# Performance work log

Measured on AMD Instinct MI355X. Metric: run time of the kernel, lower is better.

The kernel has to match this reference:

```python
import jax, jax.numpy as jnp
import numpy as np

K = 27        # num_neighs
EPS = 1e-5    # BatchNorm eps (torch default)
LATENT = 256


def _knn_idx(pts, k):
    # pts: (B, N, 3) -> (B, N, k) indices of k nearest points (self included, dist 0),
    # matching torch_cluster.knn(x, x, k).
    d = jnp.sum((pts[:, :, None, :] - pts[:, None, :, :]) ** 2, axis=-1)  # (B, N, N)
    _, idx = jax.lax.top_k(-d, k)
    return idx


def _graph_feature(x, idx):
    # x: (B, C, N), idx: (B, N, K) -> (B, 2C, N, K) = concat(neigh - center, center)
    xt = jnp.transpose(x, (0, 2, 1))               # (B, N, C)
    neigh = jax.vmap(lambda p, i: p[i])(xt, idx)   # (B, N, K, C) gather
    center = xt[:, :, None, :]                     # (B, N, 1, C)
    feat = jnp.concatenate([neigh - center, jnp.broadcast_to(center, neigh.shape)], axis=-1)
    return jnp.transpose(feat, (0, 3, 1, 2))       # (B, 2C, N, K)


def _bn_lrelu(x, gamma, beta, axes):
    # Training-mode BatchNorm (biased batch stats over `axes`, channel = dim 1) + LeakyReLU(0.2)
    mean = jnp.mean(x, axis=axes, keepdims=True)
    var = jnp.var(x, axis=axes, keepdims=True)
    shape = [1] * x.ndim
    shape[1] = -1
    y = (x - mean) * jax.lax.rsqrt(var + EPS) * gamma.reshape(shape) + beta.reshape(shape)
    return jnp.where(y >= 0, y, 0.2 * y)


def setup_inputs() -> dict:
    key = jax.random.key(0)
    ks = jax.random.split(key, 6)
    B, T, N = 2, 2, 256
    x = jax.random.normal(ks[0], (B, T, N, 3), dtype=jnp.float32)
    # Conv2d(1x1) channel ladder for depth=4, bb_size=24, input_features=6
    dims = [(6, 48), (192, 192), (768, 768), (3072, 3072)]
    inp = {"x": x}
    for i, (cin, cout) in enumerate(dims):
        inp[f"w{i}"] = jax.random.normal(ks[i + 1], (cout, cin), dtype=jnp.float32) * 0.05
        inp[f"g{i}"] = jnp.ones((cout,), jnp.float32)
        inp[f"b{i}"] = jnp.zeros((cout,), jnp.float32)
    # final Conv1d(8160 -> latent): 8160 = 48*(2+8+32+128)
    inp["w4"] = jax.random.normal(ks[5], (LATENT, 8160), dtype=jnp.float32) * 0.02
    inp["g4"] = jnp.ones((LATENT,), jnp.float32)
    inp["b4"] = jnp.zeros((LATENT,), jnp.float32)
    return inp


def reference(x, w0, g0, b0, w1, g1, b1, w2, g2, b2, w3, g3, b3, w4, g4, b4):
    B, T, N, _ = x.shape
    flat = x.reshape(B * T, N, 3)
    idx = _knn_idx(flat, K)  # fixed neighbors reused at every depth (only_true_neighs=True)
    cur = _graph_feature(jnp.transpose(flat, (0, 2, 1)), idx)  # (BT, 6, N, K)
    outs = []
    for w, g, b in [(w0, g0, b0), (w1, g1, b1), (w2, g2, b2), (w3, g3, b3)]:
        if outs:
            cur = _graph_feature(outs[-1], idx)      # (BT, 2C_prev, N, K)
        h = jnp.einsum('bcnk,oc->bonk', cur, w)      # 1x1 conv, no bias
        h = _bn_lrelu(h, g, b, axes=(0, 2, 3))
        hmax = jnp.max(h, axis=-1)                   # max over K neighbors -> (BT, C, N)
        C = hmax.shape[1]
        exp = hmax.reshape(B, T, C, N)
        # Faithful to source: avgpool does `out, _ = x.mean(dim=1, keepdim=True)` which
        # tuple-unpacks the batch dim (requires B==2): out = batch-0 temporal mean (1, C, N),
        # then expanded to (B, T, C, N).
        tp = jnp.mean(exp, axis=1, keepdims=True)[0]  # (1, C, N)
        comb = jnp.concatenate([exp, jnp.broadcast_to(tp[None], exp.shape)], axis=2)  # (B,T,2C,N)
        outs.append(comb.reshape(B * T, 2 * C, N))
    xcat = jnp.concatenate(outs, axis=1)             # (BT, 8160, N)
    y = jnp.einsum('bcn,oc->bon', xcat, w4)          # 1x1 conv1d
    y = _bn_lrelu(y, g4, b4, axes=(0, 2))
    return y.reshape(B, T, LATENT, N)
```

## Files before the change

kernel.cpp:

```cpp
#include <hip/hip_runtime.h>
#include <hip/hip_bf16.h>

#define NPTS 256
#define NB   4
#define KNN  27
#define EPSV 1e-5f

typedef unsigned short u16;
typedef _Float16 f16;
typedef __attribute__((ext_vector_type(8))) _Float16 f16x8;
typedef __attribute__((ext_vector_type(4))) _Float16 f16x4;
typedef __attribute__((ext_vector_type(4))) float f32x4;

#define OFF_IDX    0
#define OFF_XYZ    131072
#define OFF_A0     262144
#define OFF_A1     270336
#define OFF_A2     344064
#define OFF_A3     1523712
#define OFF_A4     20398080
#define OFF_PQ     24576000
#define OFF_SLICE  74907648
#define OFF_XC     100073472
#define OFF_Y      116785152

typedef __attribute__((address_space(3))) unsigned int lds_u32_t;
typedef __attribute__((address_space(1))) unsigned int glb_u32_t;

__device__ __forceinline__ void gload16(const f16* g, const u16* l) {
    __builtin_amdgcn_global_load_lds((const glb_u32_t*)g, (lds_u32_t*)(u16*)l, 16, 0, 0);
}

__device__ __forceinline__ float dist3_nocontract(float ax, float ay, float az,
                                                  float bx, float by, float bz) {
#pragma clang fp contract(off)
    float dx = bx - ax, dy = by - ay, dz = bz - az;
    float s = dx * dx;
    s = s + dy * dy;
    s = s + dz * dz;
    return s;
}

__global__ __launch_bounds__(256) void knn_prep(
    const float* __restrict__ x, int* __restrict__ idx, f16* __restrict__ xyz,
    const float* __restrict__ w0, const float* __restrict__ w1,
    const float* __restrict__ w2, const float* __restrict__ w3,
    const float* __restrict__ w4, char* __restrict__ ws)
{
    int bid = blockIdx.x;
    int tid = threadIdx.x;

    if (bid < 256) {
        int wid = tid >> 6;
        int lane = tid & 63;
        int pt = bid * 4 + wid;
        int b = pt >> 8, n = pt & 255;

        float xp0 = x[pt * 3 + 0];
        float xp1 = x[pt * 3 + 1];
        float xp2 = x[pt * 3 + 2];

        if (lane < 32) {
            float v = (lane < 3) ? x[pt * 3 + lane] : 0.f;
            xyz[((long)b * NPTS + n) * 32 + lane] = (f16)v;
        }

        unsigned long long key[4];
#pragma unroll
        for (int u = 0; u < 4; ++u) {
            int j = lane + 64 * u;
            int gj = b * NPTS + j;
            float d = dist3_nocontract(xp0, xp1, xp2,
                                       x[gj * 3 + 0], x[gj * 3 + 1], x[gj * 3 + 2]);
            key[u] = ((unsigned long long)__float_as_uint(d) << 32) | (unsigned int)j;
        }

        for (int r = 0; r < KNN; ++r) {
            unsigned long long m = key[0];
            m = key[1] < m ? key[1] : m;
            m = key[2] < m ? key[2] : m;
            m = key[3] < m ? key[3] : m;
#pragma unroll
            for (int off = 32; off; off >>= 1) {
                unsigned long long o = __shfl_xor(m, off);
                m = o < m ? o : m;
            }
            if (lane == 0) idx[pt * 28 + r] = (int)(m & 0xffffffffu);
#pragma unroll
            for (int u = 0; u < 4; ++u)
                if (key[u] == m) key[u] = ~0ULL;
        }
        return;
    }

    int pbid = bid - 256;

    if (pbid == 0) {
        f16* A = (f16*)(ws + OFF_A0);
        int jj = tid >> 2;
        int cc = (tid & 3) * 8;
        if (jj < 48) {
            f16x8 lo = {}, df = {};
#pragma unroll
            for (int j = 0; j < 8; ++j) {
                int c = cc + j;
                if (c < 3) {
                    float a = w0[jj * 6 + c];
                    float b2 = w0[jj * 6 + 3 + c];
                    lo[j] = (f16)a;
                    df[j] = (f16)(b2 - a);
                }
            }
            *(f16x8*)&A[jj * 32 + cc] = lo;
            *(f16x8*)&A[(48 + jj) * 32 + cc] = df;
        }
        if (jj < 32) {
            f16x8 z = {};
            *(f16x8*)&A[(96 + jj) * 32 + cc] = z;
        }
        return;
    }
    if (pbid < 13) {
        f16* A = (f16*)(ws + OFF_A1);
        int j = (pbid - 1) * 16 + (tid >> 4);
        int cc = (tid & 15) * 8;
        if (cc >= 96) return;
        f32x4 a0 = *(const f32x4*)&w1[j * 192 + cc];
        f32x4 a1 = *(const f32x4*)&w1[j * 192 + cc + 4];
        f32x4 b0 = *(const f32x4*)&w1[j * 192 + 96 + cc];
        f32x4 b1 = *(const f32x4*)&w1[j * 192 + 96 + cc + 4];
        f16x8 lo, df;
#pragma unroll
        for (int j2 = 0; j2 < 4; ++j2) {
            lo[j2] = (f16)a0[j2];     lo[4 + j2] = (f16)a1[j2];
            df[j2] = (f16)(b0[j2] - a0[j2]);
            df[4 + j2] = (f16)(b1[j2] - a1[j2]);
        }
        *(f16x8*)&A[j * 96 + cc] = lo;
        *(f16x8*)&A[(192 + j) * 96 + cc] = df;
        return;
    }
    if (pbid < 205) {
        f16* A = (f16*)(ws + OFF_A2);
        int j = (pbid - 13) * 4 + (tid >> 6);
        int cc = (tid & 63) * 8;
        if (cc >= 384) return;
        f32x4 a0 = *(const f32x4*)&w2[(long)j * 768 + cc];
        f32x4 a1 = *(const f32x4*)&w2[(long)j * 768 + cc + 4];
        f32x4 b0 = *(const f32x4*)&w2[(long)j * 768 + 384 + cc];
        f32x4 b1 = *(const f32x4*)&w2[(long)j * 768 + 384 + cc + 4];
        f16x8 lo, df;
#pragma unroll
        for (int j2 = 0; j2 < 4; ++j2) {
            lo[j2] = (f16)a0[j2];     lo[4 + j2] = (f16)a1[j2];
            df[j2] = (f16)(b0[j2] - a0[j2]);
            df[4 + j2] = (f16)(b1[j2] - a1[j2]);
        }
        *(f16x8*)&A[(long)j * 384 + cc] = lo;
        *(f16x8*)&A[(long)(768 + j) * 384 + cc] = df;
        return;
    }
    if (pbid < 3277) {
        f16* A = (f16*)(ws + OFF_A3);
        int j = pbid - 205;
        int cc = tid * 8;
        if (cc >= 1536) return;
        f32x4 a0 = *(const f32x4*)&w3[(long)j * 3072 + cc];
        f32x4 a1 = *(const f32x4*)&w3[(long)j * 3072 + cc + 4];
        f32x4 b0 = *(const f32x4*)&w3[(long)j * 3072 + 1536 + cc];
        f32x4 b1 = *(const f32x4*)&w3[(long)j * 3072 + 1536 + cc + 4];
        f16x8 lo, df;
#pragma unroll
        for (int j2 = 0; j2 < 4; ++j2) {
            lo[j2] = (f16)a0[j2];     lo[4 + j2] = (f16)a1[j2];
            df[j2] = (f16)(b0[j2] - a0[j2]);
            df[4 + j2] = (f16)(b1[j2] - a1[j2]);
        }
        *(f16x8*)&A[(long)j * 1536 + cc] = lo;
        *(f16x8*)&A[(long)(3072 + j) * 1536 + cc] = df;
        return;
    }
    {
        f16* A = (f16*)(ws + OFF_A4);
        int loc = pbid - 3277;
        int r = loc >> 2;
        int c0 = (loc & 3) * 2048 + tid * 8;
        if (c0 >= 8160) return;
        f32x4 a0 = *(const f32x4*)&w4[(long)r * 8160 + c0];
        f32x4 a1 = *(const f32x4*)&w4[(long)r * 8160 + c0 + 4];
        f16x8 hv;
#pragma unroll
        for (int j2 = 0; j2 < 4; ++j2) {
            hv[j2] = (f16)a0[j2];
            hv[4 + j2] = (f16)a1[j2];
        }
        *(f16x8*)&A[(long)r * 8160 + c0] = hv;
        return;
    }
}

__global__ __launch_bounds__(256) void gemm_mfma(
    const f16* __restrict__ A, const f16* __restrict__ B,
    float* __restrict__ out, int M, int Kpad, int K,
    int ldF, long bsF, long bsO, int nsplit, long pstride)
{
    __shared__ u16 sS[4][2][4096];

    int bz = blockIdx.z;
    int b = bz / nsplit, slice = bz - b * nsplit;
    int kchunk = (((K + nsplit - 1) / nsplit) + 31) & ~31;
    int kstart = slice * kchunk;
    int kend = K < kstart + kchunk ? K : kstart + kchunk;
    int nt = (kend - kstart) >> 5;

    const f16* pB = B + (long)b * bsF;
    float* Ob = out + (long)slice * pstride + (long)b * bsO;

    int m0 = blockIdx.x * 128, n0 = blockIdx.y * 128;
    int tid = threadIdx.x, lane = tid & 63, wid = tid >> 6;
    int wm = (wid >> 1) * 64, wn = (wid & 1) * 64;
    int lrow = lane & 15, quad = lane >> 4;

    int r0 = wid * 16 + (lane >> 2);
    int r1 = 64 + r0;
    int ck = lane & 3;
    int c0 = (ck ^ ((r0 >> 1) & 3)) * 8;
    int c1 = (ck ^ ((r1 >> 1) & 3)) * 8;

    const f16* gA0 = A + (long)(m0 + r0) * Kpad + c0 + kstart;
    const f16* gA1 = A + (long)(m0 + r1) * Kpad + c1 + kstart;
    const f16* gB0 = pB + (long)(n0 + r0) * ldF + c0 + kstart;
    const f16* gB1 = pB + (long)(n0 + r1) * ldF + c1 + kstart;

    int oA0 = (wid * 16) * 32;
    int oA1 = (64 + wid * 16) * 32;

    int fs = (quad ^ ((lrow >> 1) & 3)) * 8;
    int offA = (wm + lrow) * 32 + fs;
    int offB = (wn + lrow) * 32 + fs;

    f32x4 acc[4][4] = {};

#define STAGE(bf)                                                  \
    do {                                                           \
        gload16(gA0, &sS[bf][0][oA0]);                             \
        gload16(gA1, &sS[bf][0][oA1]);                             \
        gload16(gB0, &sS[bf][1][oA0]);                             \
        gload16(gB1, &sS[bf][1][oA1]);                             \
        gA0 += 32; gA1 += 32; gB0 += 32; gB1 += 32;                \
    } while (0)

    STAGE(0);
    if (nt > 1) STAGE(1);
    if (nt > 2) STAGE(2);

    for (int t = 0; t < nt; ++t) {
        int rem = nt - 1 - t;
        if (rem >= 2)      asm volatile("s_waitcnt vmcnt(8)" ::: "memory");
        else if (rem == 1) asm volatile("s_waitcnt vmcnt(4)" ::: "memory");
        else               asm volatile("s_waitcnt vmcnt(0)" ::: "memory");
        __builtin_amdgcn_s_barrier();

        if (t + 3 < nt) STAGE((t + 3) & 3);

        const u16* bA = &sS[t & 3][0][0];
        const u16* bB = &sS[t & 3][1][0];
        f16x8 fb[4];
#pragma unroll
        for (int nt4 = 0; nt4 < 4; ++nt4)
            fb[nt4] = *(const f16x8*)&bB[offB + nt4 * 512];
        __builtin_amdgcn_s_setprio(1);
#pragma unroll
        for (int mt = 0; mt < 4; ++mt) {
            f16x8 fa = *(const f16x8*)&bA[offA + mt * 512];
#pragma unroll
            for (int nt4 = 0; nt4 < 4; ++nt4)
                acc[mt][nt4] = __builtin_amdgcn_mfma_f32_16x16x32_f16(fa, fb[nt4], acc[mt][nt4], 0, 0, 0);
        }
        __builtin_amdgcn_s_setprio(0);
    }
#undef STAGE

#pragma unroll
    for (int mt = 0; mt < 4; ++mt)
#pragma unroll
        for (int nt4 = 0; nt4 < 4; ++nt4) {
            int C = n0 + wn + nt4 * 16 + lrow;
            int Rb = m0 + wm + mt * 16 + quad * 4;
#pragma unroll
            for (int r = 0; r < 4; ++r) {
                int R = Rb + r;
                if (R < M) Ob[(long)R * NPTS + C] = acc[mt][nt4][r];
            }
        }
}

__global__ __launch_bounds__(512) void gather_finalize(
    const float* __restrict__ PQ, long pstride, int nsplit,
    const int* __restrict__ idx,
    const float* __restrict__ g, const float* __restrict__ beta,
    f16* __restrict__ slice, int Co)
{
    __shared__ float p_sh[NB][NPTS];
    __shared__ float val_sh[NB][NPTS];
    __shared__ float red[2][NB][2];
    int o = blockIdx.x;
    int tid = threadIdx.x;
    int b = tid >> 7;
    int l128 = tid & 127;
    int wh = (tid >> 6) & 1;

    long ip0 = ((long)b * 2 * Co + o) * NPTS;
    long iq0 = ((long)b * 2 * Co + Co + o) * NPTS;

    float qv[2];
#pragma unroll
    for (int u = 0; u < 2; ++u) {
        int n = l128 + 128 * u;
        float v = 0.f, q = 0.f;
        for (int sp2 = 0; sp2 < nsplit; ++sp2) {
            v += PQ[sp2 * pstride + ip0 + n];
            q += PQ[sp2 * pstride + iq0 + n];
        }
        p_sh[b][n] = v;
        qv[u] = q;
    }
    __syncthreads();

#define G3(cu)                                                      \
    { float p;                                                      \
      p = p_sh[b][cu.x]; sp += p; spp = fmaf(p, p, spp);            \
      pmx = fmaxf(pmx, p); pmn = fminf(pmn, p);                     \
      p = p_sh[b][cu.y]; sp += p; spp = fmaf(p, p, spp);            \
      pmx = fmaxf(pmx, p); pmn = fminf(pmn, p);                     \
      p = p_sh[b][cu.z]; sp += p; spp = fmaf(p, p, spp);            \
      pmx = fmaxf(pmx, p); pmn = fminf(pmn, p); }
#define G4(cu)                                                      \
    { G3(cu);                                                       \
      float p = p_sh[b][cu.w]; sp += p; spp = fmaf(p, p, spp);      \
      pmx = fmaxf(pmx, p); pmn = fminf(pmn, p); }

    float mx[2], mn[2];
    float s = 0.f, ss = 0.f;
#pragma unroll
    for (int u = 0; u < 2; ++u) {
        int n = l128 + 128 * u;
        const int4* ip4 = (const int4*)(idx + ((long)b * NPTS + n) * 28);

        float sp = 0.f, spp = 0.f;
        float pmx = -__builtin_inff(), pmn = __builtin_inff();

        int4 t0 = ip4[0];
        int4 t1 = ip4[1];
        G4(t0); t0 = ip4[2];
        G4(t1); t1 = ip4[3];
        G4(t0); t0 = ip4[4];
        G4(t1); t1 = ip4[5];
        G4(t0); t0 = ip4[6];
        G4(t1);
        G3(t0);

        float q = qv[u];
        s += sp + 27.f * q;
        ss += spp + q * fmaf(2.f, sp, 27.f * q);
        mx[u] = pmx + q;
        mn[u] = pmn + q;
    }
#undef G4
#undef G3

#pragma unroll
    for (int off = 32; off; off >>= 1) {
        s += __shfl_xor(s, off);
        ss += __shfl_xor(ss, off);
    }
    if ((tid & 63) == 0) { red[0][b][wh] = s; red[1][b][wh] = ss; }
    __syncthreads();

    float ts = ((red[0][0][0] + red[0][0][1]) + (red[0][1][0] + red[0][1][1]))
             + ((red[0][2][0] + red[0][2][1]) + (red[0][3][0] + red[0][3][1]));
    float tss = ((red[1][0][0] + red[1][0][1]) + (red[1][1][0] + red[1][1][1]))
              + ((red[1][2][0] + red[1][2][1]) + (red[1][3][0] + red[1][3][1]));
    const float cnt = (float)(NB * NPTS * KNN);
    float mean = ts / cnt;
    float var = tss / cnt - mean * mean;
    float sc = g[o] * (1.0f / sqrtf(var + EPSV));
    float tt = beta[o] - mean * sc;

#pragma unroll
    for (int u = 0; u < 2; ++u) {
        int n = l128 + 128 * u;
        float v = (sc >= 0.f) ? mx[u] : mn[u];
        float z = sc * v + tt;
        val_sh[b][n] = z >= 0.f ? z : 0.2f * z;
    }
    __syncthreads();

    long ro = ((long)b * 2 * Co + o) * NPTS;
    long rt = ((long)b * 2 * Co + Co + o) * NPTS;
#pragma unroll
    for (int u = 0; u < 2; ++u) {
        int n = l128 + 128 * u;
        float tp = 0.5f * (val_sh[0][n] + val_sh[1][n]);
        slice[ro + n] = (f16)val_sh[b][n];
        slice[rt + n] = (f16)tp;
    }
}

__global__ __launch_bounds__(256) void transpose_cn(
    const f16* __restrict__ slice, f16* __restrict__ xc,
    int Ctot, int offc)
{
    __shared__ u16 t[32][36];
    int c0 = blockIdx.x * 32, n0 = blockIdx.y * 32, b = blockIdx.z;
    const f16* S = slice + (long)b * Ctot * NPTS;
    int tid = threadIdx.x;
    int r = tid >> 3, s4 = (tid & 7) * 4;

    f16x4 v = *(const f16x4*)&S[(long)(c0 + r) * NPTS + n0 + s4];
    t[r][s4 + 0] = ((const u16*)&v)[0];
    t[r][s4 + 1] = ((const u16*)&v)[1];
    t[r][s4 + 2] = ((const u16*)&v)[2];
    t[r][s4 + 3] = ((const u16*)&v)[3];
    __syncthreads();

    long base = ((long)b * NPTS + n0 + r) * 8160 + offc + c0 + s4;
    f16x4 hv;
    u16* hp = (u16*)&hv;
#pragma unroll
    for (int j = 0; j < 4; ++j) hp[j] = t[s4 + j][r];
    *(f16x4*)&xc[base] = hv;
}

__global__ __launch_bounds__(256) void final_bn(const float* __restrict__ y,
                                                const float* __restrict__ g4,
                                                const float* __restrict__ b4,
                                                float* __restrict__ out) {
    __shared__ float red[8];
    int o = blockIdx.x;
    int tid = threadIdx.x;
    int lane = tid & 63, w = tid >> 6;

    float v[4];
    float s = 0.f, ss = 0.f;
#pragma unroll
    for (int b = 0; b < 4; ++b) {
        float acc = 0.f;
#pragma unroll
        for (int sp = 0; sp < 16; ++sp)
            acc += y[sp * 262144 + b * 65536 + o * 256 + tid];
        v[b] = acc;
        s += acc;
        ss += acc * acc;
    }
#pragma unroll
    for (int off = 32; off; off >>= 1) {
        s += __shfl_xor(s, off);
        ss += __shfl_xor(ss, off);
    }
    if (lane == 0) { red[w] = s; red[4 + w] = ss; }
    __syncthreads();
    s = (red[0] + red[1]) + (red[2] + red[3]);
    ss = (red[4] + red[5]) + (red[6] + red[7]);
    float mean = s / 1024.f;
    float var = ss / 1024.f - mean * mean;
    float sc = g4[o] * (1.0f / sqrtf(var + EPSV));
    float tt = b4[o] - mean * sc;
#pragma unroll
    for (int b = 0; b < 4; ++b) {
        float z = sc * v[b] + tt;
        z = z >= 0.f ? z : 0.2f * z;
        out[(long)b * 65536 + o * 256 + tid] = z;
    }
}

extern "C" void kernel_launch(void* const* d_in, const int* in_sizes, int n_in,
                              void* d_out, int out_size, void* d_ws, size_t ws_size,
                              hipStream_t stream) {
    const float* x = (const float*)d_in[0];
    const float* wl[4];
    const float* gl[4];
    const float* bl[4];
    for (int i = 0; i < 4; ++i) {
        wl[i] = (const float*)d_in[1 + 3 * i];
        gl[i] = (const float*)d_in[2 + 3 * i];
        bl[i] = (const float*)d_in[3 + 3 * i];
    }
    const float* w4 = (const float*)d_in[13];
    const float* g4 = (const float*)d_in[14];
    const float* b4 = (const float*)d_in[15];

    char* ws = (char*)d_ws;
    int* idx = (int*)(ws + OFF_IDX);
    f16* xyz = (f16*)(ws + OFF_XYZ);
    float* PQ = (float*)(ws + OFF_PQ);
    f16* slice = (f16*)(ws + OFF_SLICE);
    f16* xc = (f16*)(ws + OFF_XC);
    float* y = (float*)(ws + OFF_Y);

    knn_prep<<<dim3(4557), dim3(256), 0, stream>>>(x, idx, xyz,
                                                   wl[0], wl[1], wl[2], wl[3], w4, ws);

    const int Kp[4] = {32, 96, 384, 1536};
    const int Co[4] = {48, 192, 768, 3072};
    const int offc[4] = {0, 96, 480, 2016};
    const int inoff[4] = {0, 0, 96, 480};
    const int nsp[4] = {1, 3, 2, 1};
    const long aoff[4] = {OFF_A0, OFF_A1, OFF_A2, OFF_A3};

    for (int i = 0; i < 4; ++i) {
        int M = 2 * Co[i];
        int Mpad = (M + 127) & ~127;
        const f16* A = (const f16*)(ws + aoff[i]);

        const f16* Bp;
        int ldF;
        long bsF;
        if (i == 0) { Bp = xyz; ldF = 32; bsF = (long)NPTS * 32; }
        else { Bp = xc + inoff[i]; ldF = 8160; bsF = (long)NPTS * 8160; }

        long pstride = (long)NB * M * NPTS;
        gemm_mfma<<<dim3(Mpad / 128, NPTS / 128, NB * nsp[i]), dim3(256), 0, stream>>>(
            A, Bp, PQ, M, Kp[i], Kp[i], ldF, bsF, (long)M * NPTS, nsp[i], pstride);

        gather_finalize<<<dim3(Co[i]), dim3(512), 0, stream>>>(
            PQ, pstride, nsp[i], idx, gl[i], bl[i], slice, Co[i]);
        transpose_cn<<<dim3(M / 32, NPTS / 32, NB), dim3(256), 0, stream>>>(
            slice, xc, M, offc[i]);
    }

    gemm_mfma<<<dim3(2, NPTS / 128, NB * 16), dim3(256), 0, stream>>>(
        (const f16*)(ws + OFF_A4), xc, y, 256, 8160, 8160, 8160,
        (long)NPTS * 8160, (long)256 * NPTS, 16, (long)NB * 256 * NPTS);
    final_bn<<<dim3(256), dim3(256), 0, stream>>>(y, g4, b4, (float*)d_out);
}
```

Before: 255.3 us.

## Fuse gather/BN finalize with transpose, writing directly into the concatenated buffer

The per-channel gather/BatchNorm/max kernel and the following transpose kernel are merged into one templated kernel. Each block now processes four output channels in sequence and writes packed f16x4 values straight into the point-major concatenation buffer. This drops one kernel launch per layer and the round trip through the intermediate slice buffer. The cost is four times fewer blocks, with each block looping serially over its channels, which lowers parallelism for the small early layers. The output stores are also strided across rows of the 8160-wide buffer.

```diff
diff --git a/kernel.cpp b/kernel.cpp
--- a/kernel.cpp
+++ b/kernel.cpp
@@ -295,37 +295,21 @@
         }
 }
 
-__global__ __launch_bounds__(512) void gather_finalize(
+template <int NO>
+__global__ __launch_bounds__(512) void gather_tx(
     const float* __restrict__ PQ, long pstride, int nsplit,
     const int* __restrict__ idx,
     const float* __restrict__ g, const float* __restrict__ beta,
-    f16* __restrict__ slice, int Co)
+    f16* __restrict__ xc, int Co, int offc)
 {
     __shared__ float p_sh[NB][NPTS];
-    __shared__ float val_sh[NB][NPTS];
+    __shared__ float val_sh[NO][NB][NPTS];
     __shared__ float red[2][NB][2];
-    int o = blockIdx.x;
+    int o0 = blockIdx.x * NO;
     int tid = threadIdx.x;
     int b = tid >> 7;
     int l128 = tid & 127;
     int wh = (tid >> 6) & 1;
-
-    long ip0 = ((long)b * 2 * Co + o) * NPTS;
-    long iq0 = ((long)b * 2 * Co + Co + o) * NPTS;
-
-    float qv[2];
-#pragma unroll
-    for (int u = 0; u < 2; ++u) {
-        int n = l128 + 128 * u;
-        float v = 0.f, q = 0.f;
-        for (int sp2 = 0; sp2 < nsplit; ++sp2) {
-            v += PQ[sp2 * pstride + ip0 + n];
-            q += PQ[sp2 * pstride + iq0 + n];
-        }
-        p_sh[b][n] = v;
-        qv[u] = q;
-    }
-    __syncthreads();
 
 #define G3(cu)                                                      \
     { float p;                                                      \
@@ -340,96 +324,103 @@
       float p = p_sh[b][cu.w]; sp += p; spp = fmaf(p, p, spp);      \
       pmx = fmaxf(pmx, p); pmn = fminf(pmn, p); }
 
-    float mx[2], mn[2];
-    float s = 0.f, ss = 0.f;
-#pragma unroll
-    for (int u = 0; u < 2; ++u) {
-        int n = l128 + 128 * u;
-        const int4* ip4 = (const int4*)(idx + ((long)b * NPTS + n) * 28);
-
-        float sp = 0.f, spp = 0.f;
-        float pmx = -__builtin_inff(), pmn = __builtin_inff();
-
-        int4 t0 = ip4[0];
-        int4 t1 = ip4[1];
-        G4(t0); t0 = ip4[2];
-        G4(t1); t1 = ip4[3];
-        G4(t0); t0 = ip4[4];
-        G4(t1); t1 = ip4[5];
-        G4(t0); t0 = ip4[6];
-        G4(t1);
-        G3(t0);
-
-        float q = qv[u];
-        s += sp + 27.f * q;
-        ss += spp + q * fmaf(2.f, sp, 27.f * q);
-        mx[u] = pmx + q;
-        mn[u] = pmn + q;
+    for (int oo = 0; oo < NO; ++oo) {
+        int o = o0 + oo;
+        long ip0 = ((long)b * 2 * Co + o) * NPTS;
+        long iq0 = ((long)b * 2 * Co + Co + o) * NPTS;
+
+        float qv[2];
+#pragma unroll
+        for (int u = 0; u < 2; ++u) {
+            int n = l128 + 128 * u;
+            float v = 0.f, q = 0.f;
+            for (int sp2 = 0; sp2 < nsplit; ++sp2) {
+                v += PQ[sp2 * pstride + ip0 + n];
+                q += PQ[sp2 * pstride + iq0 + n];
+            }
+            p_sh[b][n] = v;
+            qv[u] = q;
+        }
+        __syncthreads();
+
+        float mx[2], mn[2];
+        float s = 0.f, ss = 0.f;
+#pragma unroll
+        for (int u = 0; u < 2; ++u) {
+            int n = l128 + 128 * u;
+            const int4* ip4 = (const int4*)(idx + ((long)b * NPTS + n) * 28);
+
+            float sp = 0.f, spp = 0.f;
+            float pmx = -__builtin_inff(), pmn = __builtin_inff();
+
+            int4 t0 = ip4[0];
+            int4 t1 = ip4[1];
+            G4(t0); t0 = ip4[2];
+            G4(t1); t1 = ip4[3];
+            G4(t0); t0 = ip4[4];
+            G4(t1); t1 = ip4[5];
+            G4(t0); t0 = ip4[6];
+            G4(t1);
+            G3(t0);
+
+            float q = qv[u];
+            s += sp + 27.f * q;
+            ss += spp + q * fmaf(2.f, sp, 27.f * q);
+            mx[u] = pmx + q;
+            mn[u] = pmn + q;
+        }
+
+#pragma unroll
+        for (int off = 32; off; off >>= 1) {
+            s += __shfl_xor(s, off);
+            ss += __shfl_xor(ss, off);
+        }
+        if ((tid & 63) == 0) { red[0][b][wh] = s; red[1][b][wh] = ss; }
+        __syncthreads();
+
+        float ts = ((red[0][0][0] + red[0][0][1]) + (red[0][1][0] + red[0][1][1]))
+                 + ((red[0][2][0] + red[0][2][1]) + (red[0][3][0] + red[0][3][1]));
+        float tss = ((red[1][0][0] + red[1][0][1]) + (red[1][1][0] + red[1][1][1]))
+                  + ((red[1][2][0] + red[1][2][1]) + (red[1][3][0] + red[1][3][1]));
+        const float cnt = (float)(NB * NPTS * KNN);
+        float mean = ts / cnt;
+        float var = tss / cnt - mean * mean;
+        float sc = g[o] * (1.0f / sqrtf(var + EPSV));
+        float tt = beta[o] - mean * sc;
+
+#pragma unroll
+        for (int u = 0; u < 2; ++u) {
+            int n = l128 + 128 * u;
+            float v = (sc >= 0.f) ? mx[u] : mn[u];
+            float z = sc * v + tt;
+            val_sh[oo][b][n] = z >= 0.f ? z : 0.2f * z;
+        }
     }
 #undef G4
 #undef G3
 
-#pragma unroll
-    for (int off = 32; off; off >>= 1) {
-        s += __shfl_xor(s, off);
-        ss += __shfl_xor(ss, off);
-    }
-    if ((tid & 63) == 0) { red[0][b][wh] = s; red[1][b][wh] = ss; }
     __syncthreads();
 
-    float ts = ((red[0][0][0] + red[0][0][1]) + (red[0][1][0] + red[0][1][1]))
-             + ((red[0][2][0] + red[0][2][1]) + (red[0][3][0] + red[0][3][1]));
-    float tss = ((red[1][0][0] + red[1][0][1]) + (red[1][1][0] + red[1][1][1]))
-              + ((red[1][2][0] + red[1][2][1]) + (red[1][3][0] + red[1][3][1]));
-    const float cnt = (float)(NB * NPTS * KNN);
-    float mean = ts / cnt;
-    float var = tss / cnt - mean * mean;
-    float sc = g[o] * (1.0f / sqrtf(var + EPSV));
-    float tt = beta[o] - mean * sc;
-
 #pragma unroll
     for (int u = 0; u < 2; ++u) {
-        int n = l128 + 128 * u;
-        float v = (sc >= 0.f) ? mx[u] : mn[u];
-        float z = sc * v + tt;
-        val_sh[b][n] = z >= 0.f ? z : 0.2f * z;
-    }
-    __syncthreads();
-
-    long ro = ((long)b * 2 * Co + o) * NPTS;
-    long rt = ((long)b * 2 * Co + Co + o) * NPTS;
+        int row = u * 512 + tid;
+        int wb = row >> 8, n = row & 255;
+        f16x4 hv;
+#pragma unroll
+        for (int oo = 0; oo < NO; ++oo)
+            hv[oo] = (f16)val_sh[oo][wb][n];
+        *(f16x4*)&xc[((long)wb * NPTS + n) * 8160 + offc + o0] = hv;
+    }
 #pragma unroll
     for (int u = 0; u < 2; ++u) {
-        int n = l128 + 128 * u;
-        float tp = 0.5f * (val_sh[0][n] + val_sh[1][n]);
-        slice[ro + n] = (f16)val_sh[b][n];
-        slice[rt + n] = (f16)tp;
-    }
-}
-
-__global__ __launch_bounds__(256) void transpose_cn(
-    const f16* __restrict__ slice, f16* __restrict__ xc,
-    int Ctot, int offc)
-{
-    __shared__ u16 t[32][36];
-    int c0 = blockIdx.x * 32, n0 = blockIdx.y * 32, b = blockIdx.z;
-    const f16* S = slice + (long)b * Ctot * NPTS;
-    int tid = threadIdx.x;
-    int r = tid >> 3, s4 = (tid & 7) * 4;
-
-    f16x4 v = *(const f16x4*)&S[(long)(c0 + r) * NPTS + n0 + s4];
-    t[r][s4 + 0] = ((const u16*)&v)[0];
-    t[r][s4 + 1] = ((const u16*)&v)[1];
-    t[r][s4 + 2] = ((const u16*)&v)[2];
-    t[r][s4 + 3] = ((const u16*)&v)[3];
-    __syncthreads();
-
-    long base = ((long)b * NPTS + n0 + r) * 8160 + offc + c0 + s4;
-    f16x4 hv;
-    u16* hp = (u16*)&hv;
-#pragma unroll
-    for (int j = 0; j < 4; ++j) hp[j] = t[s4 + j][r];
-    *(f16x4*)&xc[base] = hv;
+        int row = u * 512 + tid;
+        int wb = row >> 8, n = row & 255;
+        f16x4 hv;
+#pragma unroll
+        for (int oo = 0; oo < NO; ++oo)
+            hv[oo] = (f16)(0.5f * (val_sh[oo][0][n] + val_sh[oo][1][n]));
+        *(f16x4*)&xc[((long)wb * NPTS + n) * 8160 + offc + Co + o0] = hv;
+    }
 }
 
 __global__ __launch_bounds__(256) void final_bn(const float* __restrict__ y,
@@ -494,7 +485,6 @@
     int* idx = (int*)(ws + OFF_IDX);
     f16* xyz = (f16*)(ws + OFF_XYZ);
     float* PQ = (float*)(ws + OFF_PQ);
-    f16* slice = (f16*)(ws + OFF_SLICE);
     f16* xc = (f16*)(ws + OFF_XC);
     float* y = (float*)(ws + OFF_Y);
 
@@ -523,10 +513,8 @@
         gemm_mfma<<<dim3(Mpad / 128, NPTS / 128, NB * nsp[i]), dim3(256), 0, stream>>>(
             A, Bp, PQ, M, Kp[i], Kp[i], ldF, bsF, (long)M * NPTS, nsp[i], pstride);
 
-        gather_finalize<<<dim3(Co[i]), dim3(512), 0, stream>>>(
-            PQ, pstride, nsp[i], idx, gl[i], bl[i], slice, Co[i]);
-        transpose_cn<<<dim3(M / 32, NPTS / 32, NB), dim3(256), 0, stream>>>(
-            slice, xc, M, offc[i]);
+        gather_tx<4><<<dim3(Co[i] / 4), dim3(512), 0, stream>>>(
+            PQ, pstride, nsp[i], idx, gl[i], bl[i], xc, Co[i], offc[i]);
     }
 
     gemm_mfma<<<dim3(2, NPTS / 128, NB * 16), dim3(256), 0, stream>>>(
```

Measured after the change: 334.3 us. 31.0% more time.
